# Kernel tuning notes

Measured on AMD Instinct MI355X. Metric: run time of the kernel, lower is better.

The kernel has to match this reference:

```python
import jax, jax.numpy as jnp
import numpy as np

B, T, D, M, H = 1, 256, 512, 64, 8
HD = D // H              # head_dim = 64
IN = 2 * HD + 2 * M      # crossing_net input dim = 256
HID = D // 2             # crossing_net hidden = 256


def setup_inputs() -> dict:
    key = jax.random.key(0)
    ks = jax.random.split(key, 14)
    s = 0.02
    return {
        "x": jax.random.normal(ks[0], (B, T, D), jnp.float32),
        "coords": jax.random.normal(ks[1], (B, T, M), jnp.float32),
        "Wq": jax.random.normal(ks[2], (D, D), jnp.float32) * s,
        "Wk": jax.random.normal(ks[3], (D, D), jnp.float32) * s,
        "Wv": jax.random.normal(ks[4], (D, D), jnp.float32) * s,
        "Wo": jax.random.normal(ks[5], (D, D), jnp.float32) * s,
        "W1": jax.random.normal(ks[6], (IN, HID), jnp.float32) * s,
        "b1": jnp.zeros((HID,), jnp.float32),
        "W2": jax.random.normal(ks[7], (HID, 2), jnp.float32) * s,
        "b2": jnp.zeros((2,), jnp.float32),
        "W3": jax.random.normal(ks[8], (D, D), jnp.float32) * s,
        "b3": jnp.zeros((D,), jnp.float32),
        "W4": jax.random.normal(ks[9], (D, D), jnp.float32) * s,
        "b4": jnp.zeros((D,), jnp.float32),
    }


def reference(x, coords, Wq, Wk, Wv, Wo, W1, b1, W2, b2, W3, b3, W4, b4):
    b, t, d = x.shape
    m = coords.shape[-1]
    hd = d // H
    # projections -> (B, H, T, HD)
    q = (x @ Wq).reshape(b, t, H, hd).transpose(0, 2, 1, 3)
    k = (x @ Wk).reshape(b, t, H, hd).transpose(0, 2, 1, 3)
    v = (x @ Wv).reshape(b, t, H, hd).transpose(0, 2, 1, 3)
    # crossing_net layer1 on concat([q_i, k_j, c_i, c_j]) decomposes by blocks of W1:
    W1q, W1k = W1[:hd], W1[hd:2 * hd]
    W1ci, W1cj = W1[2 * hd:2 * hd + m], W1[2 * hd + m:]
    a_i = jnp.einsum('bhid,df->bhif', q, W1q) + jnp.einsum('bim,mf->bif', coords, W1ci)[:, None]
    a_j = jnp.einsum('bhjd,df->bhjf', k, W1k) + jnp.einsum('bjm,mf->bjf', coords, W1cj)[:, None] + b1
    # (B,H,T,T,HID) pairwise hidden, then layer2 -> 2 logits
    h = jax.nn.silu(a_i[:, :, :, None, :] + a_j[:, :, None, :, :])
    z = jnp.einsum('bhijf,fc->bhijc', h, W2) + b2
    crossings = jax.nn.softmax(z, axis=-1)            # (B,H,T,T,2)
    linking = crossings[..., 0] - crossings[..., 1]   # (B,H,T,T)
    scores = linking / np.float32(np.sqrt(hd))
    causal = jnp.triu(jnp.ones((t, t), bool), 1)
    scores = jnp.where(causal, -jnp.inf, scores)
    attn = jax.nn.softmax(scores, axis=-1)
    out = jnp.einsum('bhij,bhjd->bhid', attn, v)
    out = out.transpose(0, 2, 1, 3).reshape(b, t, d)
    out = jax.nn.silu(out @ W3 + b3) @ W4 + b4        # invariant_net
    out = out @ Wo                                    # to_out
    writhe = linking.sum(axis=(-1, -2))               # (B,H)
    linking_mean = jnp.abs(linking).mean()
    return out, writhe, linking_mean
```

## Files before the change

### kernel.cpp

```cpp
#include <hip/hip_runtime.h>
#include <math.h>

#define T_ 256
#define D_ 512
#define M_ 64
#define H_ 8
#define HD_ 64
#define HID_ 256


#define SILU_ACC(acc, w, aa, bb) \
    { float t_ = (aa) + (bb); \
      float sg_ = __builtin_amdgcn_rcpf(1.f + __expf(-t_)); \
      acc = fmaf((w) * t_, sg_, acc); }

#define GEMM_INNER \
    _Pragma("unroll") \
    for (int kk = 0; kk < 32; ++kk) { \
        float a0 = As[ty * 2 + 0][kk]; \
        float a1 = As[ty * 2 + 1][kk]; \
        float b0 = Bs[kk][tx * 2 + 0]; \
        float b1 = Bs[kk][tx * 2 + 1]; \
        a00 = fmaf(a0, b0, a00); a01 = fmaf(a0, b1, a01); \
        a10 = fmaf(a1, b0, a10); a11 = fmaf(a1, b1, a11); }

__global__ __launch_bounds__(256) void k1_kernel(
    const float* __restrict__ x,
    const float* __restrict__ Wq, const float* __restrict__ Wk,
    const float* __restrict__ Wv, const float* __restrict__ W4,
    const float* __restrict__ Wo, const float* __restrict__ b4,
    float* __restrict__ y, float* __restrict__ W4o, float* __restrict__ b4o)
{
    __shared__ __align__(16) float As[32][36];
    __shared__ __align__(16) float Bs[32][36];

    const int job = blockIdx.x;
    const int tid = threadIdx.x;
    const int tx = tid & 15, ty = tid >> 4;
    const int r4 = tid >> 3, c4 = tid & 7;

    if (job < 640) {
        const float* A;
        const float* B;
        float* C;
        int row0, col0;
        if (job < 384) {
            const int z = job >> 7, rem = job & 127;
            row0 = (rem >> 4) << 5; col0 = (rem & 15) << 5;
            A = x;
            B = (z == 0) ? Wq : (z == 1) ? Wk : Wv;
            C = y + (long)z * (T_ * D_);
        } else {
            const int idx = job - 384;
            row0 = (idx >> 4) << 5; col0 = (idx & 15) << 5;
            A = W4; B = Wo; C = W4o;
        }
        float a00 = 0.f, a01 = 0.f, a10 = 0.f, a11 = 0.f;
        for (int k0 = 0; k0 < D_; k0 += 32) {
            *(float4*)&As[r4][c4 * 4] = *(const float4*)(A + (long)(row0 + r4) * D_ + k0 + c4 * 4);
            *(float4*)&Bs[r4][c4 * 4] = *(const float4*)(B + (long)(k0 + r4) * D_ + col0 + c4 * 4);
            __syncthreads();
            GEMM_INNER
            __syncthreads();
        }
        C[(long)(row0 + ty * 2 + 0) * D_ + col0 + tx * 2 + 0] = a00;
        C[(long)(row0 + ty * 2 + 0) * D_ + col0 + tx * 2 + 1] = a01;
        C[(long)(row0 + ty * 2 + 1) * D_ + col0 + tx * 2 + 0] = a10;
        C[(long)(row0 + ty * 2 + 1) * D_ + col0 + tx * 2 + 1] = a11;
    } else {
        const int c = (job - 640) * 256 + tid;
        float s = 0.f;
        for (int k = 0; k < D_; k += 4) {
            s = fmaf(b4[k + 0], Wo[(long)(k + 0) * D_ + c], s);
            s = fmaf(b4[k + 1], Wo[(long)(k + 1) * D_ + c], s);
            s = fmaf(b4[k + 2], Wo[(long)(k + 2) * D_ + c], s);
            s = fmaf(b4[k + 3], Wo[(long)(k + 3) * D_ + c], s);
        }
        b4o[c] = s;
    }
}

__global__ __launch_bounds__(256) void aiaj_kernel(
    const float* __restrict__ y, const float* __restrict__ coords,
    const float* __restrict__ W1, const float* __restrict__ b1,
    float* __restrict__ abuf)
{
    __shared__ __align__(16) float As[32][36];
    __shared__ __align__(16) float Bs[32][36];
    const int z = blockIdx.z;
    const int sel = z >> 3, h = z & 7;
    const float* Ay = y + (long)sel * (T_ * D_) + h * HD_;
    float* C = abuf + (long)z * (T_ * HID_);
    const int tid = threadIdx.x;
    const int tx = tid & 15, ty = tid >> 4;
    const int row0 = blockIdx.y * 32, col0 = blockIdx.x * 32;
    const int r4 = tid >> 3, c4 = tid & 7;
    float a00 = 0.f, a01 = 0.f, a10 = 0.f, a11 = 0.f;
    for (int k0 = 0; k0 < 128; k0 += 32) {
        if (k0 < 64) {
            *(float4*)&As[r4][c4 * 4] =
                *(const float4*)(Ay + (long)(row0 + r4) * D_ + k0 + c4 * 4);
            *(float4*)&Bs[r4][c4 * 4] =
                *(const float4*)(W1 + (long)(sel * 64 + k0 + r4) * HID_ + col0 + c4 * 4);
        } else {
            *(float4*)&As[r4][c4 * 4] =
                *(const float4*)(coords + (long)(row0 + r4) * M_ + (k0 - 64) + c4 * 4);
            *(float4*)&Bs[r4][c4 * 4] =
                *(const float4*)(W1 + (long)(128 + 64 * sel + k0 - 64 + r4) * HID_ + col0 + c4 * 4);
        }
        __syncthreads();
        GEMM_INNER
        __syncthreads();
    }
    const int c0 = col0 + tx * 2, r0 = row0 + ty * 2;
    float bb0 = (sel == 1) ? b1[c0 + 0] : 0.f;
    float bb1 = (sel == 1) ? b1[c0 + 1] : 0.f;
    C[(long)(r0 + 0) * HID_ + c0 + 0] = a00 + bb0;
    C[(long)(r0 + 0) * HID_ + c0 + 1] = a01 + bb1;
    C[(long)(r0 + 1) * HID_ + c0 + 0] = a10 + bb0;
    C[(long)(r0 + 1) * HID_ + c0 + 1] = a11 + bb1;
}

__global__ __launch_bounds__(256) void pairwise_kernel(
    const float* __restrict__ a_i, const float* __restrict__ a_j,
    const float* __restrict__ W2, float* __restrict__ pb)
{
    const int jt = blockIdx.x, it = blockIdx.y, hs = blockIdx.z;
    const int h = hs >> 2, fb = (hs & 3) * 64;
    const int t = threadIdx.x;
    __shared__ __align__(16) float ai_s[32][68];
    __shared__ __align__(16) float aj_s[32][68];
    __shared__ __align__(16) float w2d[64];
    if (t < 64) w2d[t] = W2[(fb + t) * 2 + 0] - W2[(fb + t) * 2 + 1];
    const float* aib = a_i + ((long)h * T_ + it * 32) * HID_ + fb;
    const float* ajb = a_j + ((long)h * T_ + jt * 32) * HID_ + fb;
    #pragma unroll
    for (int l = 0; l < 2; ++l) {
        int idx = t + l * 256;
        int r = idx >> 4, c4 = idx & 15;
        *(float4*)&ai_s[r][c4 * 4] = *(const float4*)(aib + (long)r * HID_ + c4 * 4);
        *(float4*)&aj_s[r][c4 * 4] = *(const float4*)(ajb + (long)r * HID_ + c4 * 4);
    }
    __syncthreads();
    const int ty = t >> 4, tx = t & 15;
    float s00 = 0.f, s01 = 0.f, s10 = 0.f, s11 = 0.f;
    #pragma unroll 4
    for (int f4 = 0; f4 < 16; ++f4) {
        float4 a0 = *(const float4*)&ai_s[ty][f4 * 4];
        float4 a1 = *(const float4*)&ai_s[ty + 16][f4 * 4];
        float4 c0 = *(const float4*)&aj_s[tx][f4 * 4];
        float4 c1 = *(const float4*)&aj_s[tx + 16][f4 * 4];
        float4 w  = *(const float4*)&w2d[f4 * 4];
        SILU_ACC(s00, w.x, a0.x, c0.x); SILU_ACC(s01, w.x, a0.x, c1.x);
        SILU_ACC(s10, w.x, a1.x, c0.x); SILU_ACC(s11, w.x, a1.x, c1.x);
        SILU_ACC(s00, w.y, a0.y, c0.y); SILU_ACC(s01, w.y, a0.y, c1.y);
        SILU_ACC(s10, w.y, a1.y, c0.y); SILU_ACC(s11, w.y, a1.y, c1.y);
        SILU_ACC(s00, w.z, a0.z, c0.z); SILU_ACC(s01, w.z, a0.z, c1.z);
        SILU_ACC(s10, w.z, a1.z, c0.z); SILU_ACC(s11, w.z, a1.z, c1.z);
        SILU_ACC(s00, w.w, a0.w, c0.w); SILU_ACC(s01, w.w, a0.w, c1.w);
        SILU_ACC(s10, w.w, a1.w, c0.w); SILU_ACC(s11, w.w, a1.w, c1.w);
    }
    const int gi0 = it * 32 + ty, gi1 = gi0 + 16;
    const int gj0 = jt * 32 + tx, gj1 = gj0 + 16;
    float* pbh = pb + (long)hs * (T_ * T_);
    pbh[(long)gi0 * T_ + gj0] = s00;
    pbh[(long)gi0 * T_ + gj1] = s01;
    pbh[(long)gi1 * T_ + gj0] = s10;
    pbh[(long)gi1 * T_ + gj1] = s11;
}

__global__ __launch_bounds__(512) void attn_kernel(
    const float* __restrict__ pb, const float* __restrict__ yv,
    const float* __restrict__ b2, float* __restrict__ o,
    float* __restrict__ parts)
{
    const int i = blockIdx.x, t = threadIdx.x;
    const int w = t >> 6, lane = t & 63;
    __shared__ float p[8][256];
    __shared__ float psc[8];
    const float b2d = b2[0] - b2[1];
    const float* pb0 = pb + ((long)(4 * w + 0) * T_ + i) * T_;
    const float* pb1 = pb + ((long)(4 * w + 1) * T_ + i) * T_;
    const float* pb2 = pb + ((long)(4 * w + 2) * T_ + i) * T_;
    const float* pb3 = pb + ((long)(4 * w + 3) * T_ + i) * T_;
    float sv[4];
    float mx = -1e30f, wsum = 0.f, asum = 0.f;
    #pragma unroll
    for (int r = 0; r < 4; ++r) {
        int j = lane + r * 64;
        float s = ((pb0[j] + pb1[j]) + (pb2[j] + pb3[j])) + b2d;
        float as = fabsf(s);
        float e = __expf(-as);
        float tv = (1.f - e) * __builtin_amdgcn_rcpf(1.f + e);
        float lk = (s < 0.f) ? -tv : tv;
        wsum += lk; asum += fabsf(lk);
        float sc = (j <= i) ? lk * 0.125f : -1e30f;
        sv[r] = sc; mx = fmaxf(mx, sc);
    }
    #pragma unroll
    for (int off = 32; off > 0; off >>= 1) mx = fmaxf(mx, __shfl_xor(mx, off));
    float sum = 0.f;
    #pragma unroll
    for (int r = 0; r < 4; ++r) {
        int j = lane + r * 64;
        float e = (j <= i) ? __expf(sv[r] - mx) : 0.f;
        p[w][j] = e; sum += e;
    }
    #pragma unroll
    for (int off = 32; off > 0; off >>= 1) {
        sum  += __shfl_xor(sum, off);
        wsum += __shfl_xor(wsum, off);
        asum += __shfl_xor(asum, off);
    }
    if (lane == 0) {
        psc[w] = __builtin_amdgcn_rcpf(sum);
        parts[((long)i * 8 + w) * 2 + 0] = wsum;
        parts[((long)i * 8 + w) * 2 + 1] = asum;
    }
    __syncthreads();
    const float pinv = psc[w];
    const float* vb = yv + t;
    float a0 = 0.f, a1 = 0.f, a2 = 0.f, a3 = 0.f;
    float a4 = 0.f, a5 = 0.f, a6 = 0.f, a7 = 0.f;
    int j = 0;
    for (; j + 7 <= i; j += 8) {
        a0 = fmaf(p[w][j + 0], vb[(long)(j + 0) * D_], a0);
        a1 = fmaf(p[w][j + 1], vb[(long)(j + 1) * D_], a1);
        a2 = fmaf(p[w][j + 2], vb[(long)(j + 2) * D_], a2);
        a3 = fmaf(p[w][j + 3], vb[(long)(j + 3) * D_], a3);
        a4 = fmaf(p[w][j + 4], vb[(long)(j + 4) * D_], a4);
        a5 = fmaf(p[w][j + 5], vb[(long)(j + 5) * D_], a5);
        a6 = fmaf(p[w][j + 6], vb[(long)(j + 6) * D_], a6);
        a7 = fmaf(p[w][j + 7], vb[(long)(j + 7) * D_], a7);
    }
    for (; j <= i; ++j) a0 = fmaf(p[w][j], vb[(long)j * D_], a0);
    o[(long)i * D_ + t] = (((a0 + a1) + (a2 + a3)) + ((a4 + a5) + (a6 + a7))) * pinv;
}

__global__ __launch_bounds__(256) void epA_kernel(
    const float* __restrict__ o, const float* __restrict__ W3,
    float* __restrict__ hbuf)
{
    __shared__ __align__(16) float As[32][36];
    __shared__ __align__(16) float Bs[32][36];
    const int z = blockIdx.z;
    float* C = hbuf + (long)z * (T_ * D_);
    const int tid = threadIdx.x;
    const int tx = tid & 15, ty = tid >> 4;
    const int row0 = blockIdx.y * 32, col0 = blockIdx.x * 32;
    const int r4 = tid >> 3, c4 = tid & 7;
    float a00 = 0.f, a01 = 0.f, a10 = 0.f, a11 = 0.f;
    for (int k0 = z * 128; k0 < z * 128 + 128; k0 += 32) {
        *(float4*)&As[r4][c4 * 4] = *(const float4*)(o + (long)(row0 + r4) * D_ + k0 + c4 * 4);
        *(float4*)&Bs[r4][c4 * 4] = *(const float4*)(W3 + (long)(k0 + r4) * D_ + col0 + c4 * 4);
        __syncthreads();
        GEMM_INNER
        __syncthreads();
    }
    C[(long)(row0 + ty * 2 + 0) * D_ + col0 + tx * 2 + 0] = a00;
    C[(long)(row0 + ty * 2 + 0) * D_ + col0 + tx * 2 + 1] = a01;
    C[(long)(row0 + ty * 2 + 1) * D_ + col0 + tx * 2 + 0] = a10;
    C[(long)(row0 + ty * 2 + 1) * D_ + col0 + tx * 2 + 1] = a11;
}

__global__ __launch_bounds__(256) void epF_kernel(
    const float* __restrict__ hbuf, const float* __restrict__ b3,
    const float* __restrict__ W4o, const float* __restrict__ b4o,
    float* __restrict__ out, const float* __restrict__ parts,
    float* __restrict__ tailo)
{
    __shared__ __align__(16) float As[32][36];
    __shared__ __align__(16) float Bs[32][36];
    const int tid = threadIdx.x;
    const int tx = tid & 15, ty = tid >> 4;
    const int row0 = blockIdx.y * 32, col0 = blockIdx.x * 32;
    const int r4 = tid >> 3, c4 = tid & 7;
    float a00 = 0.f, a01 = 0.f, a10 = 0.f, a11 = 0.f;
    for (int k0 = 0; k0 < D_; k0 += 32) {
        {
            long off = (long)(row0 + r4) * D_ + k0 + c4 * 4;
            float4 v0 = *(const float4*)(hbuf + off);
            float4 v1 = *(const float4*)(hbuf + 131072 + off);
            float4 v2 = *(const float4*)(hbuf + 262144 + off);
            float4 v3 = *(const float4*)(hbuf + 393216 + off);
            float4 bb = *(const float4*)(b3 + k0 + c4 * 4);
            float4 g;
            g.x = ((v0.x + v1.x) + (v2.x + v3.x)) + bb.x;
            g.y = ((v0.y + v1.y) + (v2.y + v3.y)) + bb.y;
            g.z = ((v0.z + v1.z) + (v2.z + v3.z)) + bb.z;
            g.w = ((v0.w + v1.w) + (v2.w + v3.w)) + bb.w;
            g.x = g.x * __builtin_amdgcn_rcpf(1.f + __expf(-g.x));
            g.y = g.y * __builtin_amdgcn_rcpf(1.f + __expf(-g.y));
            g.z = g.z * __builtin_amdgcn_rcpf(1.f + __expf(-g.z));
            g.w = g.w * __builtin_amdgcn_rcpf(1.f + __expf(-g.w));
            *(float4*)&As[r4][c4 * 4] = g;
        }
        *(float4*)&Bs[r4][c4 * 4] = *(const float4*)(W4o + (long)(k0 + r4) * D_ + col0 + c4 * 4);
        __syncthreads();
        GEMM_INNER
        __syncthreads();
    }
    const int c0 = col0 + tx * 2;
    out[(long)(row0 + ty * 2 + 0) * D_ + c0 + 0] = a00 + b4o[c0 + 0];
    out[(long)(row0 + ty * 2 + 0) * D_ + c0 + 1] = a01 + b4o[c0 + 1];
    out[(long)(row0 + ty * 2 + 1) * D_ + c0 + 0] = a10 + b4o[c0 + 0];
    out[(long)(row0 + ty * 2 + 1) * D_ + c0 + 1] = a11 + b4o[c0 + 1];

    if (blockIdx.x == 0 && blockIdx.y == 0 && tid < 64) {
        const int lane = tid;
        if (lane < 8) {
            float wsum = 0.f;
            for (int i = 0; i < 256; ++i) wsum += parts[((long)i * 8 + lane) * 2 + 0];
            tailo[lane] = wsum;
        }
        float a = 0.f;
        for (int idx = lane; idx < 2048; idx += 64) a += parts[(long)idx * 2 + 1];
        #pragma unroll
        for (int off = 32; off > 0; off >>= 1) a += __shfl_xor(a, off);
        if (lane == 0) tailo[8] = a / (float)(H_ * T_ * T_);
    }
}

extern "C" void kernel_launch(void* const* d_in, const int* in_sizes, int n_in,
                              void* d_out, int out_size, void* d_ws, size_t ws_size,
                              hipStream_t stream)
{
    const float* x      = (const float*)d_in[0];
    const float* coords = (const float*)d_in[1];
    const float* Wq     = (const float*)d_in[2];
    const float* Wk     = (const float*)d_in[3];
    const float* Wv     = (const float*)d_in[4];
    const float* Wo     = (const float*)d_in[5];
    const float* W1     = (const float*)d_in[6];
    const float* b1     = (const float*)d_in[7];
    const float* W2     = (const float*)d_in[8];
    const float* b2     = (const float*)d_in[9];
    const float* W3     = (const float*)d_in[10];
    const float* b3     = (const float*)d_in[11];
    const float* W4     = (const float*)d_in[12];
    const float* b4     = (const float*)d_in[13];
    float* out = (float*)d_out;

    float* ws = (float*)d_ws;
    float* y     = ws;
    float* ai    = ws + 393216;
    float* aj    = ws + 917504;
    float* pb    = ws + 1441792;
    float* o     = ws + 3538944;
    float* parts = ws + 3670016;
    float* W4o   = ws + 3674112;
    float* b4o   = ws + 3936256;
    float* hb    = pb;

    k1_kernel<<<dim3(642), dim3(256), 0, stream>>>(x, Wq, Wk, Wv, W4, Wo, b4,
                                                   y, W4o, b4o);

    aiaj_kernel<<<dim3(8, 8, 16), dim3(256), 0, stream>>>(y, coords, W1, b1, ai);

    pairwise_kernel<<<dim3(8, 8, 32), dim3(256), 0, stream>>>(ai, aj, W2, pb);

    attn_kernel<<<dim3(T_), dim3(512), 0, stream>>>(pb, y + 2 * (T_ * D_), b2, o, parts);

    epA_kernel<<<dim3(16, 8, 4), dim3(256), 0, stream>>>(o, W3, hb);

    epF_kernel<<<dim3(16, 8), dim3(256), 0, stream>>>(hb, b3, W4o, b4o, out,
                                                      parts, out + 131072);
}
```

Measured before the change: 117.3 us.

## Use 64x64 register-blocked tiles with 4x4 per-thread outputs in small GEMMs

Three of the dense GEMM kernels (QKV/W4·Wo projection, a_i/a_j, and the first epilogue GEMM) move from 32x32 tiles with 2x2 outputs per thread to 64x64 tiles with 4x4 float4 accumulators per thread. Shared-memory reads are vectorized and each loaded value is reused more times, which lowers LDS traffic per FMA and lets results be written with float4 stores. The trade-off is 4x fewer blocks, so grids shrink to as few as 64–160 blocks on a GPU with many CUs, which may leave compute units idle. Register pressure also rises.

```diff
diff --git a/kernel.cpp b/kernel.cpp
--- a/kernel.cpp
+++ b/kernel.cpp
@@ -13,6 +13,46 @@
     { float t_ = (aa) + (bb); \
       float sg_ = __builtin_amdgcn_rcpf(1.f + __expf(-t_)); \
       acc = fmaf((w) * t_, sg_, acc); }
+
+#define FMA4(ac, s, v) \
+    { ac.x = fmaf((s), (v).x, ac.x); ac.y = fmaf((s), (v).y, ac.y); \
+      ac.z = fmaf((s), (v).z, ac.z); ac.w = fmaf((s), (v).w, ac.w); }
+
+#define G64_STAGE_A(Aptr, lda, k0) \
+    { int f0 = tid;        int r0_ = f0 >> 3, c0_ = f0 & 7; \
+      *(float4*)&As[r0_][c0_ * 4] = \
+          *(const float4*)((Aptr) + (long)(row0 + r0_) * (lda) + (k0) + c0_ * 4); \
+      int f1 = tid + 256;  int r1_ = f1 >> 3, c1_ = f1 & 7; \
+      *(float4*)&As[r1_][c1_ * 4] = \
+          *(const float4*)((Aptr) + (long)(row0 + r1_) * (lda) + (k0) + c1_ * 4); }
+
+#define G64_STAGE_B(Bptr, ldb, k0) \
+    { int f0 = tid;        int r0_ = f0 >> 4, c0_ = f0 & 15; \
+      *(float4*)&Bs[r0_][c0_ * 4] = \
+          *(const float4*)((Bptr) + (long)((k0) + r0_) * (ldb) + col0 + c0_ * 4); \
+      int f1 = tid + 256;  int r1_ = f1 >> 4, c1_ = f1 & 15; \
+      *(float4*)&Bs[r1_][c1_ * 4] = \
+          *(const float4*)((Bptr) + (long)((k0) + r1_) * (ldb) + col0 + c1_ * 4); }
+
+#define G64_INNER \
+    _Pragma("unroll") \
+    for (int g = 0; g < 8; ++g) { \
+        float4 va0 = *(const float4*)&As[ty4 + 0][g * 4]; \
+        float4 va1 = *(const float4*)&As[ty4 + 1][g * 4]; \
+        float4 va2 = *(const float4*)&As[ty4 + 2][g * 4]; \
+        float4 va3 = *(const float4*)&As[ty4 + 3][g * 4]; \
+        float4 vb0 = *(const float4*)&Bs[g * 4 + 0][tx4]; \
+        float4 vb1 = *(const float4*)&Bs[g * 4 + 1][tx4]; \
+        float4 vb2 = *(const float4*)&Bs[g * 4 + 2][tx4]; \
+        float4 vb3 = *(const float4*)&Bs[g * 4 + 3][tx4]; \
+        FMA4(acc0, va0.x, vb0); FMA4(acc0, va0.y, vb1); \
+        FMA4(acc0, va0.z, vb2); FMA4(acc0, va0.w, vb3); \
+        FMA4(acc1, va1.x, vb0); FMA4(acc1, va1.y, vb1); \
+        FMA4(acc1, va1.z, vb2); FMA4(acc1, va1.w, vb3); \
+        FMA4(acc2, va2.x, vb0); FMA4(acc2, va2.y, vb1); \
+        FMA4(acc2, va2.z, vb2); FMA4(acc2, va2.w, vb3); \
+        FMA4(acc3, va3.x, vb0); FMA4(acc3, va3.y, vb1); \
+        FMA4(acc3, va3.z, vb2); FMA4(acc3, va3.w, vb3); }
 
 #define GEMM_INNER \
     _Pragma("unroll") \
@@ -31,44 +71,45 @@
     const float* __restrict__ Wo, const float* __restrict__ b4,
     float* __restrict__ y, float* __restrict__ W4o, float* __restrict__ b4o)
 {
-    __shared__ __align__(16) float As[32][36];
-    __shared__ __align__(16) float Bs[32][36];
+    __shared__ __align__(16) float As[64][36];
+    __shared__ __align__(16) float Bs[32][68];
 
     const int job = blockIdx.x;
     const int tid = threadIdx.x;
-    const int tx = tid & 15, ty = tid >> 4;
-    const int r4 = tid >> 3, c4 = tid & 7;
-
-    if (job < 640) {
+
+    if (job < 160) {
         const float* A;
         const float* B;
         float* C;
         int row0, col0;
-        if (job < 384) {
-            const int z = job >> 7, rem = job & 127;
-            row0 = (rem >> 4) << 5; col0 = (rem & 15) << 5;
+        if (job < 96) {
+            const int z = job >> 5, rem = job & 31;
+            row0 = (rem >> 3) << 6; col0 = (rem & 7) << 6;
             A = x;
             B = (z == 0) ? Wq : (z == 1) ? Wk : Wv;
             C = y + (long)z * (T_ * D_);
         } else {
-            const int idx = job - 384;
-            row0 = (idx >> 4) << 5; col0 = (idx & 15) << 5;
+            const int idx = job - 96;
+            row0 = (idx >> 3) << 6; col0 = (idx & 7) << 6;
             A = W4; B = Wo; C = W4o;
         }
-        float a00 = 0.f, a01 = 0.f, a10 = 0.f, a11 = 0.f;
+        const int tx4 = (tid & 15) * 4, ty4 = (tid >> 4) * 4;
+        float4 acc0 = {0, 0, 0, 0}, acc1 = {0, 0, 0, 0};
+        float4 acc2 = {0, 0, 0, 0}, acc3 = {0, 0, 0, 0};
         for (int k0 = 0; k0 < D_; k0 += 32) {
-            *(float4*)&As[r4][c4 * 4] = *(const float4*)(A + (long)(row0 + r4) * D_ + k0 + c4 * 4);
-            *(float4*)&Bs[r4][c4 * 4] = *(const float4*)(B + (long)(k0 + r4) * D_ + col0 + c4 * 4);
+            G64_STAGE_A(A, D_, k0)
+            G64_STAGE_B(B, D_, k0)
             __syncthreads();
-            GEMM_INNER
+            G64_INNER
             __syncthreads();
         }
-        C[(long)(row0 + ty * 2 + 0) * D_ + col0 + tx * 2 + 0] = a00;
-        C[(long)(row0 + ty * 2 + 0) * D_ + col0 + tx * 2 + 1] = a01;
-        C[(long)(row0 + ty * 2 + 1) * D_ + col0 + tx * 2 + 0] = a10;
-        C[(long)(row0 + ty * 2 + 1) * D_ + col0 + tx * 2 + 1] = a11;
+        const long base = (long)(row0 + ty4) * D_ + col0 + tx4;
+        *(float4*)(C + base + 0 * D_) = acc0;
+        *(float4*)(C + base + 1 * D_) = acc1;
+        *(float4*)(C + base + 2 * D_) = acc2;
+        *(float4*)(C + base + 3 * D_) = acc3;
     } else {
-        const int c = (job - 640) * 256 + tid;
+        const int c = (job - 160) * 256 + tid;
         float s = 0.f;
         for (int k = 0; k < D_; k += 4) {
             s = fmaf(b4[k + 0], Wo[(long)(k + 0) * D_ + c], s);
@@ -85,40 +126,43 @@
     const float* __restrict__ W1, const float* __restrict__ b1,
     float* __restrict__ abuf)
 {
-    __shared__ __align__(16) float As[32][36];
-    __shared__ __align__(16) float Bs[32][36];
+    __shared__ __align__(16) float As[64][36];
+    __shared__ __align__(16) float Bs[32][68];
+
     const int z = blockIdx.z;
     const int sel = z >> 3, h = z & 7;
     const float* Ay = y + (long)sel * (T_ * D_) + h * HD_;
     float* C = abuf + (long)z * (T_ * HID_);
     const int tid = threadIdx.x;
-    const int tx = tid & 15, ty = tid >> 4;
-    const int row0 = blockIdx.y * 32, col0 = blockIdx.x * 32;
-    const int r4 = tid >> 3, c4 = tid & 7;
-    float a00 = 0.f, a01 = 0.f, a10 = 0.f, a11 = 0.f;
+    const int row0 = blockIdx.y << 6, col0 = blockIdx.x << 6;
+    const int tx4 = (tid & 15) * 4, ty4 = (tid >> 4) * 4;
+
+    float4 acc0 = {0, 0, 0, 0}, acc1 = {0, 0, 0, 0};
+    float4 acc2 = {0, 0, 0, 0}, acc3 = {0, 0, 0, 0};
+
     for (int k0 = 0; k0 < 128; k0 += 32) {
         if (k0 < 64) {
-            *(float4*)&As[r4][c4 * 4] =
-                *(const float4*)(Ay + (long)(row0 + r4) * D_ + k0 + c4 * 4);
-            *(float4*)&Bs[r4][c4 * 4] =
-                *(const float4*)(W1 + (long)(sel * 64 + k0 + r4) * HID_ + col0 + c4 * 4);
+            G64_STAGE_A(Ay, D_, k0)
+            G64_STAGE_B(W1 + (long)(sel * 64) * HID_, HID_, k0)
         } else {
-            *(float4*)&As[r4][c4 * 4] =
-                *(const float4*)(coords + (long)(row0 + r4) * M_ + (k0 - 64) + c4 * 4);
-            *(float4*)&Bs[r4][c4 * 4] =
-                *(const float4*)(W1 + (long)(128 + 64 * sel + k0 - 64 + r4) * HID_ + col0 + c4 * 4);
-        }
-        __syncthreads();
-        GEMM_INNER
-        __syncthreads();
-    }
-    const int c0 = col0 + tx * 2, r0 = row0 + ty * 2;
-    float bb0 = (sel == 1) ? b1[c0 + 0] : 0.f;
-    float bb1 = (sel == 1) ? b1[c0 + 1] : 0.f;
-    C[(long)(r0 + 0) * HID_ + c0 + 0] = a00 + bb0;
-    C[(long)(r0 + 0) * HID_ + c0 + 1] = a01 + bb1;
-    C[(long)(r0 + 1) * HID_ + c0 + 0] = a10 + bb0;
-    C[(long)(r0 + 1) * HID_ + c0 + 1] = a11 + bb1;
+            G64_STAGE_A(coords, M_, k0 - 64)
+            G64_STAGE_B(W1 + (long)(128 + 64 * sel) * HID_, HID_, k0 - 64)
+        }
+        __syncthreads();
+        G64_INNER
+        __syncthreads();
+    }
+    float4 bb = {0, 0, 0, 0};
+    if (sel == 1) bb = *(const float4*)(b1 + col0 + tx4);
+    acc0.x += bb.x; acc0.y += bb.y; acc0.z += bb.z; acc0.w += bb.w;
+    acc1.x += bb.x; acc1.y += bb.y; acc1.z += bb.z; acc1.w += bb.w;
+    acc2.x += bb.x; acc2.y += bb.y; acc2.z += bb.z; acc2.w += bb.w;
+    acc3.x += bb.x; acc3.y += bb.y; acc3.z += bb.z; acc3.w += bb.w;
+    const long base = (long)(row0 + ty4) * HID_ + col0 + tx4;
+    *(float4*)(C + base + 0 * HID_) = acc0;
+    *(float4*)(C + base + 1 * HID_) = acc1;
+    *(float4*)(C + base + 2 * HID_) = acc2;
+    *(float4*)(C + base + 3 * HID_) = acc3;
 }
 
 __global__ __launch_bounds__(256) void pairwise_kernel(
@@ -241,26 +285,30 @@
     const float* __restrict__ o, const float* __restrict__ W3,
     float* __restrict__ hbuf)
 {
-    __shared__ __align__(16) float As[32][36];
-    __shared__ __align__(16) float Bs[32][36];
-    const int z = blockIdx.z;
-    float* C = hbuf + (long)z * (T_ * D_);
+    __shared__ __align__(16) float As[64][36];
+    __shared__ __align__(16) float Bs[32][68];
+
+    const int ks = blockIdx.z;
+    float* C = hbuf + (long)ks * (T_ * D_);
     const int tid = threadIdx.x;
-    const int tx = tid & 15, ty = tid >> 4;
-    const int row0 = blockIdx.y * 32, col0 = blockIdx.x * 32;
-    const int r4 = tid >> 3, c4 = tid & 7;
-    float a00 = 0.f, a01 = 0.f, a10 = 0.f, a11 = 0.f;
-    for (int k0 = z * 128; k0 < z * 128 + 128; k0 += 32) {
-        *(float4*)&As[r4][c4 * 4] = *(const float4*)(o + (long)(row0 + r4) * D_ + k0 + c4 * 4);
-        *(float4*)&Bs[r4][c4 * 4] = *(const float4*)(W3 + (long)(k0 + r4) * D_ + col0 + c4 * 4);
-        __syncthreads();
-        GEMM_INNER
-        __syncthreads();
-    }
-    C[(long)(row0 + ty * 2 + 0) * D_ + col0 + tx * 2 + 0] = a00;
-    C[(long)(row0 + ty * 2 + 0) * D_ + col0 + tx * 2 + 1] = a01;
-    C[(long)(row0 + ty * 2 + 1) * D_ + col0 + tx * 2 + 0] = a10;
-    C[(long)(row0 + ty * 2 + 1) * D_ + col0 + tx * 2 + 1] = a11;
+    const int row0 = blockIdx.y << 6, col0 = blockIdx.x << 6;
+    const int tx4 = (tid & 15) * 4, ty4 = (tid >> 4) * 4;
+
+    float4 acc0 = {0, 0, 0, 0}, acc1 = {0, 0, 0, 0};
+    float4 acc2 = {0, 0, 0, 0}, acc3 = {0, 0, 0, 0};
+
+    for (int k0 = ks * 128; k0 < ks * 128 + 128; k0 += 32) {
+        G64_STAGE_A(o, D_, k0)
+        G64_STAGE_B(W3, D_, k0)
+        __syncthreads();
+        G64_INNER
+        __syncthreads();
+    }
+    const long base = (long)(row0 + ty4) * D_ + col0 + tx4;
+    *(float4*)(C + base + 0 * D_) = acc0;
+    *(float4*)(C + base + 1 * D_) = acc1;
+    *(float4*)(C + base + 2 * D_) = acc2;
+    *(float4*)(C + base + 3 * D_) = acc3;
 }
 
 __global__ __launch_bounds__(256) void epF_kernel(
@@ -352,16 +400,16 @@
     float* b4o   = ws + 3936256;
     float* hb    = pb;
 
-    k1_kernel<<<dim3(642), dim3(256), 0, stream>>>(x, Wq, Wk, Wv, W4, Wo, b4,
+    k1_kernel<<<dim3(162), dim3(256), 0, stream>>>(x, Wq, Wk, Wv, W4, Wo, b4,
                                                    y, W4o, b4o);
 
-    aiaj_kernel<<<dim3(8, 8, 16), dim3(256), 0, stream>>>(y, coords, W1, b1, ai);
+    aiaj_kernel<<<dim3(4, 4, 16), dim3(256), 0, stream>>>(y, coords, W1, b1, ai);
 
     pairwise_kernel<<<dim3(8, 8, 32), dim3(256), 0, stream>>>(ai, aj, W2, pb);
 
     attn_kernel<<<dim3(T_), dim3(512), 0, stream>>>(pb, y + 2 * (T_ * D_), b2, o, parts);
 
-    epA_kernel<<<dim3(16, 8, 4), dim3(256), 0, stream>>>(o, W3, hb);
+    epA_kernel<<<dim3(8, 4, 4), dim3(256), 0, stream>>>(o, W3, hb);
 
     epF_kernel<<<dim3(16, 8), dim3(256), 0, stream>>>(hb, b3, W4o, b4o, out,
                                                       parts, out + 131072);
```

Result: slower. 121.4 us (+3.5%).
